# Optimization experiments

Hardware: AMD Instinct MI355X
Metric: run time of the kernel (lower is better)

## Reference

```python
import jax, jax.numpy as jnp
import numpy as np

NH, NKV, HD = 32, 8, 128   # query heads, kv heads, head_dim
EPS = 1e-6
ROPE_BASE = 10000.0


def setup_inputs() -> dict:
    key = jax.random.key(0)
    ks = jax.random.split(key, 5)
    B, S, H = 2, 1024, 4096
    scale = 0.02
    return {
        "x": jax.random.normal(ks[0], (B, S, H), jnp.float32),
        "wq": jax.random.normal(ks[1], (H, NH * HD), jnp.float32) * scale,
        "wk": jax.random.normal(ks[2], (H, NKV * HD), jnp.float32) * scale,
        "wv": jax.random.normal(ks[3], (H, NKV * HD), jnp.float32) * scale,
        "wo": jax.random.normal(ks[4], (NH * HD, H), jnp.float32) * scale,
        "q_norm_w": jnp.ones((HD,), jnp.float32),
        "k_norm_w": jnp.ones((HD,), jnp.float32),
    }


def _rmsnorm(t, w):
    # per-head RMSNorm over last dim (head_dim)
    var = jnp.mean(t * t, axis=-1, keepdims=True)
    return t * jax.lax.rsqrt(var + EPS) * w


def _rope(t, cos, sin):
    # t: [B,S,h,d]; cos/sin: [S, d/2] (neox / rotate-half style)
    d2 = t.shape[-1] // 2
    t1, t2 = t[..., :d2], t[..., d2:]
    c = cos[None, :, None, :]
    s = sin[None, :, None, :]
    return jnp.concatenate([t1 * c - t2 * s, t1 * s + t2 * c], axis=-1)


def reference(x, wq, wk, wv, wo, q_norm_w, k_norm_w):
    B, S, H = x.shape
    softmax_scale = HD ** (-0.5)

    q = (x @ wq).reshape(B, S, NH, HD)
    k = (x @ wk).reshape(B, S, NKV, HD)
    v = (x @ wv).reshape(B, S, NKV, HD)

    # QK RMSNorm (qwen3 use_qk_norm)
    q = _rmsnorm(q, q_norm_w)
    k = _rmsnorm(k, k_norm_w)

    # rotary embedding, base 10000
    inv_freq = 1.0 / (ROPE_BASE ** (jnp.arange(0, HD, 2, dtype=jnp.float32) / HD))
    ang = jnp.arange(S, dtype=jnp.float32)[:, None] * inv_freq[None, :]  # [S, d/2]
    cos, sin = jnp.cos(ang), jnp.sin(ang)
    q = _rope(q, cos, sin)
    k = _rope(k, cos, sin)

    # GQA: expand kv heads to match query heads
    g = NH // NKV
    k = jnp.repeat(k, g, axis=2)  # [B,S,NH,HD]
    v = jnp.repeat(v, g, axis=2)

    scores = jnp.einsum("bqhd,bkhd->bhqk", q, k) * softmax_scale
    causal = jnp.tril(jnp.ones((S, S), dtype=bool))
    scores = jnp.where(causal[None, None], scores, jnp.finfo(scores.dtype).min)
    probs = jax.nn.softmax(scores, axis=-1)
    ctx = jnp.einsum("bhqk,bkhd->bqhd", probs, v).reshape(B, S, NH * HD)
    return ctx @ wo
```

## Files before the change

kernel.cpp:

```cpp
#include <hip/hip_runtime.h>


#define NH_ 32
#define NKV_ 8
#define HD_ 128
#define SEQ_ 1024
#define HID_ 4096
#define NQKV_ 6144

typedef unsigned short u16;
typedef __bf16 bf16x8 __attribute__((ext_vector_type(8)));
typedef float f32x4 __attribute__((ext_vector_type(4)));

__device__ __forceinline__ u16 f2bf(float f) {
  unsigned int u = __float_as_uint(f);
  return (u16)((u + 0x7FFFu + ((u >> 16) & 1u)) >> 16);
}
__device__ __forceinline__ float bf2f(u16 u) {
  return __uint_as_float(((unsigned int)u) << 16);
}
__device__ __forceinline__ f32x4 mfma16(bf16x8 a, bf16x8 b, f32x4 c) {
  return __builtin_amdgcn_mfma_f32_16x16x32_bf16(a, b, c, 0, 0, 0);
}
__device__ __forceinline__ void gld16(u16* lds, const u16* g) {
  __builtin_amdgcn_global_load_lds(
      (const __attribute__((address_space(1))) unsigned int*)g,
      (__attribute__((address_space(3))) unsigned int*)lds, 16, 0, 0);
}

__global__ __launch_bounds__(256) void prep_all(
    const float* __restrict__ x, const float* __restrict__ wq,
    const float* __restrict__ wk, const float* __restrict__ wv,
    u16* __restrict__ xb, u16* __restrict__ wqkvt) {
  const int blk = blockIdx.x;
  if (blk < 4096) {
    int i = (blk * 256 + threadIdx.x) * 8;
    float4 a = *(const float4*)(x + i);
    float4 b = *(const float4*)(x + i + 4);
    u16 o[8];
    o[0] = f2bf(a.x); o[1] = f2bf(a.y); o[2] = f2bf(a.z); o[3] = f2bf(a.w);
    o[4] = f2bf(b.x); o[5] = f2bf(b.y); o[6] = f2bf(b.z); o[7] = f2bf(b.w);
    *(uint4*)(xb + i) = *(uint4*)&o[0];
    return;
  }
  __shared__ float t[32][33];
  const int tt = blk - 4096;
  const int k0 = (tt & 127) * 32;
  const int y = tt >> 7;
  const float* src;
  int ldn, n0;
  size_t dofs;
  if (y < 128) { src = wq; ldn = 4096; n0 = y * 32; dofs = 0; }
  else if (y < 160) { src = wk; ldn = 1024; n0 = (y - 128) * 32; dofs = (size_t)4096 * 4096; }
  else { src = wv; ldn = 1024; n0 = (y - 160) * 32; dofs = (size_t)5120 * 4096; }
  const int c = threadIdx.x & 31, r4 = threadIdx.x >> 5;
#pragma unroll
  for (int i = 0; i < 4; ++i) {
    int r = r4 + i * 8;
    t[r][c] = src[(size_t)(k0 + r) * ldn + n0 + c];
  }
  __syncthreads();
#pragma unroll
  for (int i = 0; i < 4; ++i) {
    int r = r4 + i * 8;
    wqkvt[dofs + (size_t)(n0 + r) * HID_ + k0 + c] = f2bf(t[c][r]);
  }
}

__global__ __launch_bounds__(256) void mid_all(
    const float* __restrict__ wo, const u16* __restrict__ QKV,
    const float* __restrict__ QW, const float* __restrict__ KW,
    u16* __restrict__ wot, u16* __restrict__ QB, u16* __restrict__ KB,
    u16* __restrict__ VT) {
  const int blk = blockIdx.x;
  if (blk < 16384) {
    __shared__ float t[32][33];
    const int k0 = (blk & 127) * 32, n0 = (blk >> 7) * 32;
    const int c = threadIdx.x & 31, r4 = threadIdx.x >> 5;
#pragma unroll
    for (int i = 0; i < 4; ++i) {
      int r = r4 + i * 8;
      t[r][c] = wo[(size_t)(k0 + r) * HID_ + n0 + c];
    }
    __syncthreads();
#pragma unroll
    for (int i = 0; i < 4; ++i) {
      int r = r4 + i * 8;
      wot[(size_t)(n0 + r) * HID_ + k0 + c] = f2bf(t[c][r]);
    }
    return;
  }
  if (blk < 36864) {
    const float QSCALE = 0.08838834764831845f * 1.4426950408889634f;
    int vec = (blk - 16384) * 4 + (threadIdx.x >> 6);
    int lane = threadIdx.x & 63;
    const u16* src;
    u16* dst;
    const float* nw;
    int m;
    float outsc;
    if (vec < 65536) {
      m = vec >> 5;
      int hh = vec & 31;
      src = QKV + (size_t)m * NQKV_ + hh * 128;
      int b = m >> 10, s = m & 1023;
      dst = QB + (size_t)((b * NH_ + hh) * SEQ_ + s) * HD_;
      nw = QW;
      outsc = QSCALE;
    } else {
      int vk = vec - 65536;
      m = vk >> 3;
      int kvh = vk & 7;
      src = QKV + (size_t)m * NQKV_ + 4096 + kvh * 128;
      int b = m >> 10, s = m & 1023;
      dst = KB + (size_t)((b * NKV_ + kvh) * SEQ_ + s) * HD_;
      nw = KW;
      outsc = 1.0f;
    }
    float t1 = bf2f(src[lane]), t2 = bf2f(src[lane + 64]);
    float ss = t1 * t1 + t2 * t2;
#pragma unroll
    for (int off = 32; off >= 1; off >>= 1) ss += __shfl_xor(ss, off);
    float scale = rsqrtf(ss * (1.0f / 128.0f) + 1e-6f) * outsc;
    float n1 = t1 * scale * nw[lane];
    float n2 = t2 * scale * nw[lane + 64];
    int spos = m & 1023;
    float invf = powf(10000.0f, -(float)lane * (1.0f / 64.0f));
    float ang = (float)spos * invf;
    float sn, cs;
    sincosf(ang, &sn, &cs);
    dst[lane] = f2bf(n1 * cs - n2 * sn);
    dst[lane + 64] = f2bf(n1 * sn + n2 * cs);
    return;
  }
  {
    __shared__ u16 t[32][33];
    const int tt = blk - 36864;
    const int s0 = (tt & 31) * 32, d0 = ((tt >> 5) & 3) * 32;
    const int bkvh = tt >> 7;
    const int b = bkvh >> 3, kvh = bkvh & 7;
    const int c = threadIdx.x & 31, r8 = threadIdx.x >> 5;
#pragma unroll
    for (int i = 0; i < 4; ++i) {
      int r = r8 + i * 8;
      t[r][c] =
          QKV[(size_t)(b * SEQ_ + s0 + r) * NQKV_ + 5120 + kvh * 128 + d0 + c];
    }
    __syncthreads();
#pragma unroll
    for (int i = 0; i < 4; ++i) {
      int r = r8 + i * 8;
      VT[(size_t)(bkvh * HD_ + d0 + r) * SEQ_ + s0 + c] = t[c][r];
    }
  }
}


#define BAR() __builtin_amdgcn_s_barrier()
#define PRIO1() __builtin_amdgcn_s_setprio(1)
#define PRIO0() __builtin_amdgcn_s_setprio(0)
#define LGKM0() asm volatile("s_waitcnt lgkmcnt(0)" ::: "memory")
#define VM(n) asm volatile("s_waitcnt vmcnt(" #n ")" ::: "memory")

#define STGA(slot, l, koff) \
  gld16(&L[(slot)*SLOT + (l)*4096 + wofs], aB + (size_t)(l)*64*K + (koff))
#define STGB(slot, l, koff) \
  gld16(&L[(slot)*SLOT + 8192 + (l)*4096 + wofs], bB + (size_t)(l)*64*K + (koff))

#define RDB(Ls, p)                                                        \
  bq[0][0] = *(const bf16x8*)&(Ls)[bro + (2*(p))*4096 + acS0];            \
  bq[0][1] = *(const bf16x8*)&(Ls)[bro + (2*(p)+1)*4096 + acS0];          \
  bq[1][0] = *(const bf16x8*)&(Ls)[bro + (2*(p))*4096 + acS1];            \
  bq[1][1] = *(const bf16x8*)&(Ls)[bro + (2*(p)+1)*4096 + acS1];

#define RDA(Ls)                                                           \
  _Pragma("unroll") for (int m_ = 0; m_ < 4; ++m_) {                      \
    af[0][m_] = *(const bf16x8*)&(Ls)[aro + m_*1024 + acS0];              \
    af[1][m_] = *(const bf16x8*)&(Ls)[aro + m_*1024 + acS1];              \
  }

#define MMp(p)                                                            \
  _Pragma("unroll") for (int kk = 0; kk < 2; ++kk)                        \
  _Pragma("unroll") for (int m = 0; m < 4; ++m)                           \
  _Pragma("unroll") for (int j = 0; j < 2; ++j)                           \
    acc[m][2*(p)+j] = mfma16(af[kk][m], bq[kk][j], acc[m][2*(p)+j]);

template <int NF, bool F32OUT>
__global__ __launch_bounds__(512, 2) void gemm3p(
    const u16* __restrict__ A_, const u16* __restrict__ Bt,
    void* __restrict__ Cv, const int K, const int ldc) {
  constexpr int NSLOT = (NF == 4) ? 3 : 2;
  constexpr int SLOT = (2 + NF) * 4096;
  __shared__ __align__(16) u16 L[NSLOT * SLOT];

  const int sw = (blockIdx.x & 7) * 32 + (blockIdx.x >> 3);
  const int bm = sw >> 4, bn = sw & 15;

  const int tid = threadIdx.x, w = tid >> 6, lane = tid & 63;
  const int wm = w >> 2, wn = w & 3;
  const int ln = lane & 15, quad = lane >> 4;

  const int srow = lane >> 3;
  const int scol = ((lane & 7) ^ srow) * 8;
  const u16* aB = A_ + (size_t)(bm * 128 + w * 8 + srow) * K + scol;
  const u16* bB = Bt + (size_t)(bn * (NF * 64) + w * 8 + srow) * K + scol;
  const int wofs = w * 512;

  const int acS0 = (quad * 8) ^ ((ln & 7) << 3);
  const int acS1 = (32 + quad * 8) ^ ((ln & 7) << 3);
  const int aro = (wm * 64 + ln) * 64;
  const int bro = 8192 + (wn * 16 + ln) * 64;

  f32x4 acc[4][NF];
#pragma unroll
  for (int m = 0; m < 4; ++m)
#pragma unroll
    for (int f = 0; f < NF; ++f)
#pragma unroll
      for (int r = 0; r < 4; ++r) acc[m][f][r] = 0.0f;

  const int nt = K >> 6;
  bf16x8 af[2][4], bq[2][2];

  if constexpr (NF == 6) {
    STGA(0, 0, 0); STGA(0, 1, 0);
    STGB(0, 0, 0); STGB(0, 1, 0); STGB(0, 2, 0);
    STGB(0, 3, 0); STGB(0, 4, 0); STGB(0, 5, 0);
    VM(4); BAR();
#pragma unroll 1
    for (int t = 0; t < nt - 1; ++t) {
      const u16* Ls = &L[(t & 1) * SLOT];
      const int sn = (t + 1) & 1;
      const int k1 = (t + 1) << 6;
      RDA(Ls); RDB(Ls, 0);
      STGA(sn, 0, k1); STGA(sn, 1, k1); STGB(sn, 0, k1); STGB(sn, 1, k1);
      BAR(); LGKM0(); PRIO1(); MMp(0); PRIO0(); VM(6); BAR();
      RDB(Ls, 1);
      STGB(sn, 2, k1); STGB(sn, 3, k1);
      BAR(); LGKM0(); PRIO1(); MMp(1); PRIO0(); VM(6); BAR();
      RDB(Ls, 2);
      STGB(sn, 4, k1); STGB(sn, 5, k1);
      BAR(); LGKM0(); PRIO1(); MMp(2); PRIO0(); VM(4); BAR();
    }
    {
      const u16* Ls = &L[((nt - 1) & 1) * SLOT];
      RDA(Ls); RDB(Ls, 0);
      BAR(); LGKM0(); PRIO1(); MMp(0); PRIO0(); VM(2); BAR();
      RDB(Ls, 1);
      BAR(); LGKM0(); PRIO1(); MMp(1); PRIO0(); VM(0); BAR();
      RDB(Ls, 2);
      BAR(); LGKM0(); PRIO1(); MMp(2); PRIO0();
    }
  } else {
    STGA(0, 0, 0); STGA(0, 1, 0);
    STGB(0, 0, 0); STGB(0, 1, 0); STGB(0, 2, 0); STGB(0, 3, 0);
    STGA(1, 0, 64); STGA(1, 1, 64);
    STGB(1, 0, 64); STGB(1, 1, 64); STGB(1, 2, 64); STGB(1, 3, 64);
    VM(6); BAR();
    int so = 0;
#pragma unroll 1
    for (int t = 0; t < nt - 2; ++t) {
      const u16* Ls = &L[so * SLOT];
      const int sn = (so == 0) ? 2 : so - 1;
      const int k2 = (t + 2) << 6;
      RDA(Ls); RDB(Ls, 0);
      STGA(sn, 0, k2); STGA(sn, 1, k2); STGB(sn, 0, k2); STGB(sn, 1, k2);
      BAR(); LGKM0(); PRIO1(); MMp(0); PRIO0(); BAR();
      RDB(Ls, 1);
      STGB(sn, 2, k2); STGB(sn, 3, k2);
      BAR(); LGKM0(); PRIO1(); MMp(1); PRIO0(); VM(6); BAR();
      so = (so == 2) ? 0 : so + 1;
    }
    {
      const u16* Ls = &L[so * SLOT];
      RDA(Ls); RDB(Ls, 0);
      BAR(); LGKM0(); PRIO1(); MMp(0); PRIO0(); BAR();
      RDB(Ls, 1);
      BAR(); LGKM0(); PRIO1(); MMp(1); PRIO0(); VM(0); BAR();
      so = (so == 2) ? 0 : so + 1;
    }
    {
      const u16* Ls = &L[so * SLOT];
      RDA(Ls); RDB(Ls, 0);
      BAR(); LGKM0(); PRIO1(); MMp(0); PRIO0(); BAR();
      RDB(Ls, 1);
      BAR(); LGKM0(); PRIO1(); MMp(1); PRIO0();
    }
  }

  const int colb = bn * (NF * 64) + wn * 16 + ln;
#pragma unroll
  for (int m = 0; m < 4; ++m) {
#pragma unroll
    for (int r = 0; r < 4; ++r) {
      const int grow = bm * 128 + wm * 64 + m * 16 + quad * 4 + r;
      if (F32OUT) {
        float* dst = (float*)Cv + (size_t)grow * ldc + colb;
#pragma unroll
        for (int f = 0; f < NF; ++f) dst[f * 64] = acc[m][f][r];
      } else {
        u16* dst = (u16*)Cv + (size_t)grow * ldc + colb;
#pragma unroll
        for (int f = 0; f < NF; ++f) dst[f * 64] = f2bf(acc[m][f][r]);
      }
    }
  }
}

#undef RDB
#undef RDA
#undef MMp
#undef STGA
#undef STGB
#undef BAR
#undef PRIO1
#undef PRIO0
#undef LGKM0
#undef VM

__global__ __launch_bounds__(256) void flash_attn(
    const u16* __restrict__ QB, const u16* __restrict__ KB,
    const u16* __restrict__ VT, u16* __restrict__ CTX) {
  __shared__ u16 Ks[4][64][32];
  __shared__ u16 Vs[2][128][32];
  __shared__ u16 Pl[4][16][72];

  const int bid = blockIdx.x;
  const int qt = 15 - (bid >> 6);
  const int h = bid & 31, b = (bid >> 5) & 1;
  const int kvh = h >> 2;
  const int tid = threadIdx.x, w = tid >> 6, lane = tid & 63;
  const int ln = lane & 15, quad = lane >> 4;
  const int l4 = lane >> 2, l4r = lane & 3;

  const u16* qbase =
      QB + (size_t)((b * NH_ + h) * SEQ_ + qt * 64 + w * 16 + ln) * HD_;
  bf16x8 qf[4];
#pragma unroll
  for (int kc = 0; kc < 4; ++kc)
    qf[kc] = *(const bf16x8*)(qbase + kc * 32 + quad * 8);

  f32x4 o[8];
#pragma unroll
  for (int t = 0; t < 8; ++t)
#pragma unroll
    for (int r = 0; r < 4; ++r) o[t][r] = 0.0f;
  float m_r[4] = {-3e38f, -3e38f, -3e38f, -3e38f};
  float l_r[4] = {0.0f, 0.0f, 0.0f, 0.0f};

  const u16* krow =
      KB + (size_t)((b * NKV_ + kvh) * SEQ_ + w * 16 + l4) * HD_ + l4r * 8;
  const u16* vrow =
      VT + (size_t)((b * NKV_ + kvh) * HD_ + w * 32 + l4) * SEQ_ + l4r * 8;
  const int pswz = ((ln >> 3) & 1) << 3;

  for (int kt = 0; kt <= qt; ++kt) {
    const int key0 = kt * 64;
#pragma unroll
    for (int i = 0; i < 4; ++i)
      gld16(&Ks[i][w * 16][0], krow + (size_t)key0 * HD_ + i * 32);
#pragma unroll
    for (int i = 0; i < 4; ++i)
      gld16(&Vs[i & 1][w * 32 + (i >> 1) * 16][0],
            vrow + (size_t)(i >> 1) * 16 * SEQ_ + key0 + (i & 1) * 32);
    __syncthreads();

    f32x4 sc[4];
#pragma unroll
    for (int t2 = 0; t2 < 4; ++t2) {
#pragma unroll
      for (int r = 0; r < 4; ++r) sc[t2][r] = 0.0f;
#pragma unroll
      for (int kc = 0; kc < 4; ++kc) {
        bf16x8 kf = *(const bf16x8*)&Ks[kc][t2 * 16 + ln][quad * 8];
        sc[t2] = mfma16(qf[kc], kf, sc[t2]);
      }
    }

    const bool diag = (kt == qt);
    float p[4][4], alpha[4];
#pragma unroll
    for (int r = 0; r < 4; ++r) {
      float s0 = sc[0][r], s1 = sc[1][r], s2 = sc[2][r], s3 = sc[3][r];
      if (diag) {
        const int qi = qt * 64 + w * 16 + quad * 4 + r;
        if (key0 + ln > qi) s0 = -3e38f;
        if (key0 + 16 + ln > qi) s1 = -3e38f;
        if (key0 + 32 + ln > qi) s2 = -3e38f;
        if (key0 + 48 + ln > qi) s3 = -3e38f;
      }
      float mx = fmaxf(fmaxf(s0, s1), fmaxf(s2, s3));
#pragma unroll
      for (int off = 1; off < 16; off <<= 1) mx = fmaxf(mx, __shfl_xor(mx, off));
      float mnew = fmaxf(m_r[r], mx);
      alpha[r] = exp2f(m_r[r] - mnew);
      p[0][r] = exp2f(s0 - mnew);
      p[1][r] = exp2f(s1 - mnew);
      p[2][r] = exp2f(s2 - mnew);
      p[3][r] = exp2f(s3 - mnew);
      float rs = p[0][r] + p[1][r] + p[2][r] + p[3][r];
#pragma unroll
      for (int off = 1; off < 16; off <<= 1) rs += __shfl_xor(rs, off);
      l_r[r] = l_r[r] * alpha[r] + rs;
      m_r[r] = mnew;
    }
#pragma unroll
    for (int t = 0; t < 8; ++t)
#pragma unroll
      for (int r = 0; r < 4; ++r) o[t][r] *= alpha[r];

#pragma unroll
    for (int r = 0; r < 4; ++r) {
      const int row = quad * 4 + r;
      const int wswz = ((row >> 3) & 1) << 3;
#pragma unroll
      for (int t2 = 0; t2 < 4; ++t2)
        Pl[w][row][(t2 * 16 + ln) ^ wswz] = f2bf(p[t2][r]);
    }
    bf16x8 af0 = *(const bf16x8*)&Pl[w][ln][(quad * 8) ^ pswz];
    bf16x8 af1 = *(const bf16x8*)&Pl[w][ln][32 + ((quad * 8) ^ pswz)];
#pragma unroll
    for (int t = 0; t < 8; ++t) {
      bf16x8 vf0 = *(const bf16x8*)&Vs[0][t * 16 + ln][quad * 8];
      o[t] = mfma16(af0, vf0, o[t]);
      bf16x8 vf1 = *(const bf16x8*)&Vs[1][t * 16 + ln][quad * 8];
      o[t] = mfma16(af1, vf1, o[t]);
    }
    __syncthreads();
  }

#pragma unroll
  for (int r = 0; r < 4; ++r) {
    float inv_l = 1.0f / l_r[r];
    int srow = qt * 64 + w * 16 + quad * 4 + r;
    u16* dst = CTX + (size_t)(b * SEQ_ + srow) * (NH_ * HD_) + h * HD_;
#pragma unroll
    for (int t = 0; t < 8; ++t) dst[t * 16 + ln] = f2bf(o[t][r] * inv_l);
  }
}

extern "C" void kernel_launch(void* const* d_in, const int* in_sizes, int n_in,
                              void* d_out, int out_size, void* d_ws,
                              size_t ws_size, hipStream_t stream) {
  const float* x = (const float*)d_in[0];
  const float* wq = (const float*)d_in[1];
  const float* wk = (const float*)d_in[2];
  const float* wv = (const float*)d_in[3];
  const float* wo = (const float*)d_in[4];
  const float* qw = (const float*)d_in[5];
  const float* kw = (const float*)d_in[6];
  float* out = (float*)d_out;
  char* ws = (char*)d_ws;
  const size_t MB = 1024 * 1024;

  u16* wqkvt = (u16*)ws;
  u16* wot = (u16*)ws;
  u16* xb = (u16*)(ws + 48 * MB);
  u16* qkv = (u16*)(ws + 64 * MB);
  u16* ctx = (u16*)(ws + 64 * MB);
  u16* qb = (u16*)(ws + 88 * MB);
  u16* kb = (u16*)(ws + 104 * MB);
  u16* vt = (u16*)(ws + 108 * MB);

  prep_all<<<dim3(28672), 256, 0, stream>>>(x, wq, wk, wv, xb, wqkvt);
  gemm3p<6, false><<<dim3(256), 512, 0, stream>>>(xb, wqkvt, qkv, 4096, 6144);
  mid_all<<<dim3(38912), 256, 0, stream>>>(wo, qkv, qw, kw, wot, qb, kb, vt);
  flash_attn<<<dim3(1024), 256, 0, stream>>>(qb, kb, vt, ctx);
  gemm3p<4, true><<<dim3(256), 512, 0, stream>>>(ctx, wot, out, 4096, 4096);
}
```

Before: 454.3 us.

## Double-buffer K/V tiles in flash attention and raise MFMA wave priority

The flash attention loop now prefetches the next K/V tile into a second LDS buffer while computing on the current one. This hides global-to-LDS load latency behind the QK and PV MFMAs, at the cost of doubled LDS use for K/V, which may lower occupancy. MFMA sections are wrapped in s_setprio raises. The RoPE inverse frequency now uses exp2f instead of powf.

```diff
diff --git a/kernel.cpp b/kernel.cpp
--- a/kernel.cpp
+++ b/kernel.cpp
@@ -125,7 +125,7 @@
     float n1 = t1 * scale * nw[lane];
     float n2 = t2 * scale * nw[lane + 64];
     int spos = m & 1023;
-    float invf = powf(10000.0f, -(float)lane * (1.0f / 64.0f));
+    float invf = exp2f((float)lane * -0.20762050593046f);
     float ang = (float)spos * invf;
     float sn, cs;
     sincosf(ang, &sn, &cs);
@@ -154,7 +154,6 @@
     }
   }
 }
-
 
 #define BAR() __builtin_amdgcn_s_barrier()
 #define PRIO1() __builtin_amdgcn_s_setprio(1)
@@ -312,17 +311,12 @@
 #undef MMp
 #undef STGA
 #undef STGB
-#undef BAR
-#undef PRIO1
-#undef PRIO0
-#undef LGKM0
-#undef VM
 
 __global__ __launch_bounds__(256) void flash_attn(
     const u16* __restrict__ QB, const u16* __restrict__ KB,
     const u16* __restrict__ VT, u16* __restrict__ CTX) {
-  __shared__ u16 Ks[4][64][32];
-  __shared__ u16 Vs[2][128][32];
+  __shared__ u16 Ks[2][4][64][32];
+  __shared__ u16 Vs[2][2][128][32];
   __shared__ u16 Pl[4][16][72];
 
   const int bid = blockIdx.x;
@@ -354,28 +348,34 @@
       VT + (size_t)((b * NKV_ + kvh) * HD_ + w * 32 + l4) * SEQ_ + l4r * 8;
   const int pswz = ((ln >> 3) & 1) << 3;
 
+#define STAGEKV(d_, k0_)                                                    \
+  _Pragma("unroll") for (int i = 0; i < 4; ++i)                             \
+      gld16(&Ks[d_][i][w * 16][0], krow + (size_t)(k0_)*HD_ + i * 32);      \
+  _Pragma("unroll") for (int i = 0; i < 4; ++i)                             \
+      gld16(&Vs[d_][i & 1][w * 32 + (i >> 1) * 16][0],                      \
+            vrow + (size_t)(i >> 1) * 16 * SEQ_ + (k0_) + (i & 1) * 32);
+
+  STAGEKV(0, 0);
+  __syncthreads();
+
   for (int kt = 0; kt <= qt; ++kt) {
     const int key0 = kt * 64;
-#pragma unroll
-    for (int i = 0; i < 4; ++i)
-      gld16(&Ks[i][w * 16][0], krow + (size_t)key0 * HD_ + i * 32);
-#pragma unroll
-    for (int i = 0; i < 4; ++i)
-      gld16(&Vs[i & 1][w * 32 + (i >> 1) * 16][0],
-            vrow + (size_t)(i >> 1) * 16 * SEQ_ + key0 + (i & 1) * 32);
-    __syncthreads();
+    const int d = kt & 1;
+    if (kt < qt) { STAGEKV(d ^ 1, key0 + 64); }
 
     f32x4 sc[4];
+    PRIO1();
 #pragma unroll
     for (int t2 = 0; t2 < 4; ++t2) {
 #pragma unroll
       for (int r = 0; r < 4; ++r) sc[t2][r] = 0.0f;
 #pragma unroll
       for (int kc = 0; kc < 4; ++kc) {
-        bf16x8 kf = *(const bf16x8*)&Ks[kc][t2 * 16 + ln][quad * 8];
+        bf16x8 kf = *(const bf16x8*)&Ks[d][kc][t2 * 16 + ln][quad * 8];
         sc[t2] = mfma16(qf[kc], kf, sc[t2]);
       }
     }
+    PRIO0();
 
     const bool diag = (kt == qt);
     float p[4][4], alpha[4];
@@ -419,15 +419,18 @@
     }
     bf16x8 af0 = *(const bf16x8*)&Pl[w][ln][(quad * 8) ^ pswz];
     bf16x8 af1 = *(const bf16x8*)&Pl[w][ln][32 + ((quad * 8) ^ pswz)];
+    PRIO1();
 #pragma unroll
     for (int t = 0; t < 8; ++t) {
-      bf16x8 vf0 = *(const bf16x8*)&Vs[0][t * 16 + ln][quad * 8];
+      bf16x8 vf0 = *(const bf16x8*)&Vs[d][0][t * 16 + ln][quad * 8];
       o[t] = mfma16(af0, vf0, o[t]);
-      bf16x8 vf1 = *(const bf16x8*)&Vs[1][t * 16 + ln][quad * 8];
+      bf16x8 vf1 = *(const bf16x8*)&Vs[d][1][t * 16 + ln][quad * 8];
       o[t] = mfma16(af1, vf1, o[t]);
     }
+    PRIO0();
     __syncthreads();
   }
+#undef STAGEKV
 
 #pragma unroll
   for (int r = 0; r < 4; ++r) {
@@ -438,6 +441,12 @@
     for (int t = 0; t < 8; ++t) dst[t * 16 + ln] = f2bf(o[t][r] * inv_l);
   }
 }
+
+#undef BAR
+#undef PRIO1
+#undef PRIO0
+#undef LGKM0
+#undef VM
 
 extern "C" void kernel_launch(void* const* d_in, const int* in_sizes, int n_in,
                               void* d_out, int out_size, void* d_ws,
```

After: 455.5 us. Within noise of the previous version (+0.3%).
